# Optimization experiments

Hardware: AMD Instinct MI355X
Metric: run time of the kernel (lower is better)

The kernel has to match this reference:

```python
import jax, jax.numpy as jnp
import numpy as np
from jax import lax

RES = 2048
MAX_VAL = 1.0
COST_SCALE = 0.01
N_ITERS = 10
BOUNDARY_FRAC = 0.02  # sparse scattered Dirichlet cells, realistic for a planner occupancy grid


def _neighbor_sum(V):
    # replicate-pad (zero-Neumann at the outer border), 4-point stencil sum
    Vp = jnp.pad(V, 1, mode='edge')
    return Vp[:-2, 1:-1] + Vp[2:, 1:-1] + Vp[1:-1, :-2] + Vp[1:-1, 2:]


def setup_inputs() -> dict:
    key = jax.random.key(0)
    k1, k2, k3, k4 = jax.random.split(key, 4)
    x = jax.random.uniform(k1, (RES, RES), jnp.float32)
    # sparse boundary/obstacle cells (boundary_types > 0 means Dirichlet cell)
    boundary_types = (jax.random.uniform(k2, (RES, RES)) < BOUNDARY_FRAC).astype(jnp.int32)
    boundary_conditions = jax.random.uniform(k3, (RES, RES), jnp.float32)
    # learnable cost field, initialized around cost_scale (some negatives so ReLU matters)
    C = COST_SCALE + COST_SCALE * jax.random.normal(k4, (RES, RES), jnp.float32)
    return {'x': x, 'C': C, 'boundary_types': boundary_types,
            'boundary_conditions': boundary_conditions}


def reference(x, C, boundary_types, boundary_conditions):
    mask = boundary_types > 0
    # inject boundary conditions into the initial potential (x[obj_inds] = bc[obj_inds])
    V = jnp.where(mask, boundary_conditions, x)
    C_pos = jax.nn.relu(C)
    denom = 4.0 + C_pos  # screened Laplace: (4 + C) V = sum(neighbors)

    def step(V, _):
        V_new = _neighbor_sum(V) / denom
        V_new = jnp.where(mask, boundary_conditions, V_new)
        return V_new, None

    V, _ = lax.scan(step, V, None, length=N_ITERS)

    out = jnp.where(V >= MAX_VAL, 0.95 * MAX_VAL, V)
    out = jnp.where(mask, boundary_conditions, out)
    return out, C_pos
```

## Files before the change

### kernel.cpp

```cpp
#include <hip/hip_runtime.h>


#define RES    2048
#define XHALO  12
#define YHALO  10
#define DIMX   128
#define DIMY   64
#define OUTX   (DIMX - 2*XHALO)
#define OUTY   (DIMY - 2*YHALO)
#define NBX    ((RES + OUTX - 1) / OUTX)
#define NBY    ((RES + OUTY - 1) / OUTY)
#define NWG    (NBX*NBY)
#define NITER  10

__global__ __launch_bounds__(512, 4)
void laplace10_fused(const float* __restrict__ Xin,
                     const float* __restrict__ Cin,
                     const float* __restrict__ BTf,
                     const float* __restrict__ BCin,
                     float* __restrict__ OUT,
                     float* __restrict__ CPOS) {
  __shared__ __align__(16) float V[2][DIMY][DIMX];

  const int t  = threadIdx.x;
  const int q  = t & 31;
  const int ty = t >> 5;
  const int x0 = q * 4;
  const int y0 = ty * 4;

  int wg = (int)blockIdx.x;
  {
    const int qq = NWG / 8, rr = NWG % 8;
    const int xcd = wg % 8, off = wg / 8;
    wg = (xcd < rr ? xcd * (qq + 1) : rr * (qq + 1) + (xcd - rr) * qq) + off;
  }
  const int bx  = wg % NBX, by = wg / NBX;
  const int tx0 = bx * OUTX - XHALO;
  const int ty0 = by * OUTY - YHALO;
  const int gx0 = tx0 + x0;

  const bool xfull = (gx0 >= 0) && (gx0 + 4 <= RES);
  const int  xcl   = (gx0 < 0) ? 0 : (RES - 1);
  const bool xin   = xfull && (x0 >= XHALO) && (x0 < XHALO + OUTX);

  auto load4 = [&](const float* __restrict__ g, int row) -> float4 {
    if (xfull) return *(const float4*)(g + (size_t)row * RES + gx0);
    const float v = g[(size_t)row * RES + xcl];
    return make_float4(v, v, v, v);
  };

  const bool lq0 = (gx0 + 0 <= 0);
  const bool lq1 = (gx0 + 1 <= 0);
  const bool lq2 = (gx0 + 2 <= 0);
  const bool lq3 = (gx0 + 3 <= 0);
  const bool rq0 = (gx0 + 0 >= RES - 1);
  const bool rq1 = (gx0 + 1 >= RES - 1);
  const bool rq2 = (gx0 + 2 >= RES - 1);
  const bool rq3 = (gx0 + 3 >= RES - 1);

  unsigned mb = 0u;
  float4 Bq[4], Rq[4], cur[4];
#pragma unroll
  for (int j = 0; j < 4; ++j) {
    const int yy = y0 + j;
    const int g  = ty0 + yy;
    const int gc = g < 0 ? 0 : (g > RES - 1 ? RES - 1 : g);
    const float4 mv = load4(BTf, gc);
    const float4 bv = load4(BCin, gc);
    const float4 cv = load4(Cin, gc);
    const float4 xv = load4(Xin, gc);
    const unsigned m0 = (__float_as_uint(mv.x) != 0u);
    const unsigned m1 = (__float_as_uint(mv.y) != 0u);
    const unsigned m2 = (__float_as_uint(mv.z) != 0u);
    const unsigned m3 = (__float_as_uint(mv.w) != 0u);
    mb |= (m0 | (m1 << 1) | (m2 << 2) | (m3 << 3)) << (4 * j);
    float4 B;
    B.x = m0 ? bv.x : 0.0f;  B.y = m1 ? bv.y : 0.0f;
    B.z = m2 ? bv.z : 0.0f;  B.w = m3 ? bv.w : 0.0f;
    Bq[j] = B;
    float4 cp;
    cp.x = cv.x > 0.0f ? cv.x : 0.0f;
    cp.y = cv.y > 0.0f ? cv.y : 0.0f;
    cp.z = cv.z > 0.0f ? cv.z : 0.0f;
    cp.w = cv.w > 0.0f ? cv.w : 0.0f;
    float4 R;
    R.x = m0 ? 0.0f : 1.0f / (4.0f + cp.x);
    R.y = m1 ? 0.0f : 1.0f / (4.0f + cp.y);
    R.z = m2 ? 0.0f : 1.0f / (4.0f + cp.z);
    R.w = m3 ? 0.0f : 1.0f / (4.0f + cp.w);
    Rq[j] = R;
    float4 v0;
    v0.x = m0 ? B.x : xv.x;  v0.y = m1 ? B.y : xv.y;
    v0.z = m2 ? B.z : xv.z;  v0.w = m3 ? B.w : xv.w;
    cur[j] = v0;
    *(float4*)(&V[0][yy][x0]) = v0;
    if (xin && yy >= YHALO && yy < YHALO + OUTY && g < RES) {
      *(float4*)(CPOS + (size_t)g * RES + gx0) = cp;
    }
  }
  __syncthreads();

  const int ytop = (ty == 0)  ? 0        : y0 - 1;
  const int ybot = (ty == 15) ? DIMY - 1 : y0 + 4;

  #define ROW_STEP(J, VP, VM, VN, NV)                                          \
    {                                                                          \
      const int g_ = ty0 + y0 + (J);                                           \
      const float lf = __shfl((VM).w, (t + 63) & 63);                          \
      const float rt = __shfl((VM).x, (t + 1) & 63);                           \
      const float4 va = (g_ <= 0)       ? (VM) : (VP);                         \
      const float4 vb = (g_ >= RES - 1) ? (VM) : (VN);                         \
      const float n0 = va.x + vb.x + (lq0 ? (VM).x : lf)     + (rq0 ? (VM).x : (VM).y); \
      const float n1 = va.y + vb.y + (lq1 ? (VM).y : (VM).x) + (rq1 ? (VM).y : (VM).z); \
      const float n2 = va.z + vb.z + (lq2 ? (VM).z : (VM).y) + (rq2 ? (VM).z : (VM).w); \
      const float n3 = va.w + vb.w + (lq3 ? (VM).w : (VM).z) + (rq3 ? (VM).w : rt);     \
      (NV).x = fmaf(n0, Rq[J].x, Bq[J].x);                                     \
      (NV).y = fmaf(n1, Rq[J].y, Bq[J].y);                                     \
      (NV).z = fmaf(n2, Rq[J].z, Bq[J].z);                                     \
      (NV).w = fmaf(n3, Rq[J].w, Bq[J].w);                                     \
    }

#pragma unroll 1
  for (int it = 1; it < NITER; ++it) {
    const float* const src = &V[(it + 1) & 1][0][0];
    float* const dst       = &V[it & 1][0][0];
    const float4 top = *(const float4*)(src + ytop * DIMX + x0);
    const float4 bot = *(const float4*)(src + ybot * DIMX + x0);
    float4 n0v, n1v, n2v, n3v;
    ROW_STEP(0, top,    cur[0], cur[1], n0v);
    ROW_STEP(1, cur[0], cur[1], cur[2], n1v);
    ROW_STEP(2, cur[1], cur[2], cur[3], n2v);
    ROW_STEP(3, cur[2], cur[3], bot,    n3v);
    cur[0] = n0v; cur[1] = n1v; cur[2] = n2v; cur[3] = n3v;
    *(float4*)(dst + (y0 + 0) * DIMX + x0) = n0v;
    *(float4*)(dst + (y0 + 1) * DIMX + x0) = n1v;
    *(float4*)(dst + (y0 + 2) * DIMX + x0) = n2v;
    *(float4*)(dst + (y0 + 3) * DIMX + x0) = n3v;
    __syncthreads();
  }

  {
    const float* const src = &V[1][0][0];
    const float4 top = *(const float4*)(src + ytop * DIMX + x0);
    const float4 bot = *(const float4*)(src + ybot * DIMX + x0);
    float4 n0v, n1v, n2v, n3v;
    ROW_STEP(0, top,    cur[0], cur[1], n0v);
    ROW_STEP(1, cur[0], cur[1], cur[2], n1v);
    ROW_STEP(2, cur[1], cur[2], cur[3], n2v);
    ROW_STEP(3, cur[2], cur[3], bot,    n3v);
    cur[0] = n0v; cur[1] = n1v; cur[2] = n2v; cur[3] = n3v;
#pragma unroll
    for (int j = 0; j < 4; ++j) {
      const int yy = y0 + j;
      const int g  = ty0 + yy;
      if (xin && yy >= YHALO && yy < YHALO + OUTY && g < RES) {
        const float4 nv = cur[j];
        float4 o;
        o.x = (nv.x >= 1.0f) ? 0.95f : nv.x;
        o.y = (nv.y >= 1.0f) ? 0.95f : nv.y;
        o.z = (nv.z >= 1.0f) ? 0.95f : nv.z;
        o.w = (nv.w >= 1.0f) ? 0.95f : nv.w;
        *(float4*)(OUT + (size_t)g * RES + gx0) = o;
      }
    }
  }
  #undef ROW_STEP
}

extern "C" void kernel_launch(void* const* d_in, const int* in_sizes, int n_in,
                              void* d_out, int out_size, void* d_ws, size_t ws_size,
                              hipStream_t stream) {
  const float* Xin  = (const float*)d_in[0];
  const float* Cin  = (const float*)d_in[1];
  const float* BTf  = (const float*)d_in[2];
  const float* BCin = (const float*)d_in[3];
  float* OUT  = (float*)d_out;
  float* CPOS = OUT + (size_t)RES * RES;

  hipLaunchKernelGGL(laplace10_fused, dim3(NWG), dim3(512), 0, stream,
                     Xin, Cin, BTf, BCin, OUT, CPOS);
}
```

Measured before the change: 131.1 us.

## Exchange stencil halos via wave shuffles and small LDS buffer; specialize interior tiles

Replaces the full double-buffered 64x128 LDS tile with a small halo buffer: rows shared between the two half-waves of a wavefront are exchanged with cross-lane shuffles, and only rows crossing wavefront boundaries go through LDS. Interior workgroups use a template specialization that drops all boundary clamping logic. The lower LDS footprint allows raising launch bounds to 8 blocks per CU, and the iteration loop is fully unrolled. This increases register pressure, which could limit the occupancy gain.

```diff
diff --git a/kernel.cpp b/kernel.cpp
--- a/kernel.cpp
+++ b/kernel.cpp
@@ -12,68 +12,64 @@
 #define NBY    ((RES + OUTY - 1) / OUTY)
 #define NWG    (NBX*NBY)
 #define NITER  10
-
-__global__ __launch_bounds__(512, 4)
-void laplace10_fused(const float* __restrict__ Xin,
-                     const float* __restrict__ Cin,
-                     const float* __restrict__ BTf,
-                     const float* __restrict__ BCin,
-                     float* __restrict__ OUT,
-                     float* __restrict__ CPOS) {
-  __shared__ __align__(16) float V[2][DIMY][DIMX];
-
-  const int t  = threadIdx.x;
-  const int q  = t & 31;
-  const int ty = t >> 5;
-  const int x0 = q * 4;
-  const int y0 = ty * 4;
-
-  int wg = (int)blockIdx.x;
-  {
-    const int qq = NWG / 8, rr = NWG % 8;
-    const int xcd = wg % 8, off = wg / 8;
-    wg = (xcd < rr ? xcd * (qq + 1) : rr * (qq + 1) + (xcd - rr) * qq) + off;
-  }
-  const int bx  = wg % NBX, by = wg / NBX;
-  const int tx0 = bx * OUTX - XHALO;
-  const int ty0 = by * OUTY - YHALO;
-  const int gx0 = tx0 + x0;
-
-  const bool xfull = (gx0 >= 0) && (gx0 + 4 <= RES);
-  const int  xcl   = (gx0 < 0) ? 0 : (RES - 1);
+#define HSTRIDE (8*2*DIMX)
+
+using HaloT = float[2][8][2][DIMX];
+
+template<bool EDGE>
+__device__ __forceinline__ void body(const int t, const int bx, const int by,
+    const float* __restrict__ Xin, const float* __restrict__ Cin,
+    const float* __restrict__ BTf, const float* __restrict__ BCin,
+    float* __restrict__ OUT, float* __restrict__ CPOS, HaloT& H)
+{
+  const int  q      = t & 31;
+  const int  ty     = t >> 5;
+  const int  w      = t >> 6;
+  const bool tyEven = (ty & 1) == 0;
+  const int  x0     = q * 4;
+  const int  y0     = ty * 4;
+  const int  tx0    = bx * OUTX - XHALO;
+  const int  ty0    = by * OUTY - YHALO;
+  const int  gx0    = tx0 + x0;
+  const int  gyr    = ty0 + y0;
+
+  const bool xfull = !EDGE || ((gx0 >= 0) && (gx0 + 4 <= RES));
   const bool xin   = xfull && (x0 >= XHALO) && (x0 < XHALO + OUTX);
 
+  const bool lq0 = EDGE && (gx0 + 0 <= 0);
+  const bool lq1 = EDGE && (gx0 + 1 <= 0);
+  const bool lq2 = EDGE && (gx0 + 2 <= 0);
+  const bool lq3 = EDGE && (gx0 + 3 <= 0);
+  const bool rq0 = EDGE && (gx0 + 0 >= RES - 1);
+  const bool rq1 = EDGE && (gx0 + 1 >= RES - 1);
+  const bool rq2 = EDGE && (gx0 + 2 >= RES - 1);
+  const bool rq3 = EDGE && (gx0 + 3 >= RES - 1);
+
   auto load4 = [&](const float* __restrict__ g, int row) -> float4 {
-    if (xfull) return *(const float4*)(g + (size_t)row * RES + gx0);
-    const float v = g[(size_t)row * RES + xcl];
-    return make_float4(v, v, v, v);
+    if constexpr (EDGE) {
+      if (xfull) return *(const float4*)(g + (size_t)row * RES + gx0);
+      const int xc = (gx0 < 0) ? 0 : (RES - 1);
+      const float v = g[(size_t)row * RES + xc];
+      return make_float4(v, v, v, v);
+    } else {
+      return *(const float4*)(g + (size_t)row * RES + gx0);
+    }
   };
 
-  const bool lq0 = (gx0 + 0 <= 0);
-  const bool lq1 = (gx0 + 1 <= 0);
-  const bool lq2 = (gx0 + 2 <= 0);
-  const bool lq3 = (gx0 + 3 <= 0);
-  const bool rq0 = (gx0 + 0 >= RES - 1);
-  const bool rq1 = (gx0 + 1 >= RES - 1);
-  const bool rq2 = (gx0 + 2 >= RES - 1);
-  const bool rq3 = (gx0 + 3 >= RES - 1);
-
-  unsigned mb = 0u;
   float4 Bq[4], Rq[4], cur[4];
 #pragma unroll
   for (int j = 0; j < 4; ++j) {
     const int yy = y0 + j;
-    const int g  = ty0 + yy;
-    const int gc = g < 0 ? 0 : (g > RES - 1 ? RES - 1 : g);
+    const int g  = gyr + j;
+    const int gc = EDGE ? (g < 0 ? 0 : (g > RES - 1 ? RES - 1 : g)) : g;
     const float4 mv = load4(BTf, gc);
     const float4 bv = load4(BCin, gc);
     const float4 cv = load4(Cin, gc);
     const float4 xv = load4(Xin, gc);
-    const unsigned m0 = (__float_as_uint(mv.x) != 0u);
-    const unsigned m1 = (__float_as_uint(mv.y) != 0u);
-    const unsigned m2 = (__float_as_uint(mv.z) != 0u);
-    const unsigned m3 = (__float_as_uint(mv.w) != 0u);
-    mb |= (m0 | (m1 << 1) | (m2 << 2) | (m3 << 3)) << (4 * j);
+    const bool m0 = __float_as_uint(mv.x) != 0u;
+    const bool m1 = __float_as_uint(mv.y) != 0u;
+    const bool m2 = __float_as_uint(mv.z) != 0u;
+    const bool m3 = __float_as_uint(mv.w) != 0u;
     float4 B;
     B.x = m0 ? bv.x : 0.0f;  B.y = m1 ? bv.y : 0.0f;
     B.z = m2 ? bv.z : 0.0f;  B.w = m3 ? bv.w : 0.0f;
@@ -93,78 +89,100 @@
     v0.x = m0 ? B.x : xv.x;  v0.y = m1 ? B.y : xv.y;
     v0.z = m2 ? B.z : xv.z;  v0.w = m3 ? B.w : xv.w;
     cur[j] = v0;
-    *(float4*)(&V[0][yy][x0]) = v0;
-    if (xin && yy >= YHALO && yy < YHALO + OUTY && g < RES) {
+    if (xin && yy >= YHALO && yy < YHALO + OUTY && (!EDGE || g < RES)) {
       *(float4*)(CPOS + (size_t)g * RES + gx0) = cp;
     }
   }
+
+  const int wr = tyEven ? (w > 0 ? w - 1 : 0) : (w < 7 ? w + 1 : 7);
+  float* const       hw = &H[0][w][tyEven ? 0 : 1][x0];
+  const float* const hr = &H[0][wr][tyEven ? 1 : 0][x0];
+  *(float4*)hw = tyEven ? cur[0] : cur[3];
   __syncthreads();
 
-  const int ytop = (ty == 0)  ? 0        : y0 - 1;
-  const int ybot = (ty == 15) ? DIMY - 1 : y0 + 4;
-
-  #define ROW_STEP(J, VP, VM, VN, NV)                                          \
-    {                                                                          \
-      const int g_ = ty0 + y0 + (J);                                           \
-      const float lf = __shfl((VM).w, (t + 63) & 63);                          \
-      const float rt = __shfl((VM).x, (t + 1) & 63);                           \
-      const float4 va = (g_ <= 0)       ? (VM) : (VP);                         \
-      const float4 vb = (g_ >= RES - 1) ? (VM) : (VN);                         \
-      const float n0 = va.x + vb.x + (lq0 ? (VM).x : lf)     + (rq0 ? (VM).x : (VM).y); \
-      const float n1 = va.y + vb.y + (lq1 ? (VM).y : (VM).x) + (rq1 ? (VM).y : (VM).z); \
-      const float n2 = va.z + vb.z + (lq2 ? (VM).z : (VM).y) + (rq2 ? (VM).z : (VM).w); \
-      const float n3 = va.w + vb.w + (lq3 ? (VM).w : (VM).z) + (rq3 ? (VM).w : rt);     \
-      (NV).x = fmaf(n0, Rq[J].x, Bq[J].x);                                     \
-      (NV).y = fmaf(n1, Rq[J].y, Bq[J].y);                                     \
-      (NV).z = fmaf(n2, Rq[J].z, Bq[J].z);                                     \
-      (NV).w = fmaf(n3, Rq[J].w, Bq[J].w);                                     \
-    }
-
-#pragma unroll 1
-  for (int it = 1; it < NITER; ++it) {
-    const float* const src = &V[(it + 1) & 1][0][0];
-    float* const dst       = &V[it & 1][0][0];
-    const float4 top = *(const float4*)(src + ytop * DIMX + x0);
-    const float4 bot = *(const float4*)(src + ybot * DIMX + x0);
-    float4 n0v, n1v, n2v, n3v;
-    ROW_STEP(0, top,    cur[0], cur[1], n0v);
-    ROW_STEP(1, cur[0], cur[1], cur[2], n1v);
-    ROW_STEP(2, cur[1], cur[2], cur[3], n2v);
-    ROW_STEP(3, cur[2], cur[3], bot,    n3v);
-    cur[0] = n0v; cur[1] = n1v; cur[2] = n2v; cur[3] = n3v;
-    *(float4*)(dst + (y0 + 0) * DIMX + x0) = n0v;
-    *(float4*)(dst + (y0 + 1) * DIMX + x0) = n1v;
-    *(float4*)(dst + (y0 + 2) * DIMX + x0) = n2v;
-    *(float4*)(dst + (y0 + 3) * DIMX + x0) = n3v;
-    __syncthreads();
-  }
-
+  auto rowstep = [&](int gy, const float4 R, const float4 B,
+                     const float4 vp, const float4 vm, const float4 vn) -> float4 {
+    const float lf = __shfl(vm.w, (t + 63) & 63);
+    const float rt = __shfl(vm.x, (t + 1) & 63);
+    float4 nv;
+    if constexpr (EDGE) {
+      const float4 va = (gy <= 0)       ? vm : vp;
+      const float4 vb = (gy >= RES - 1) ? vm : vn;
+      nv.x = fmaf(va.x + vb.x + (lq0 ? vm.x : lf)   + (rq0 ? vm.x : vm.y), R.x, B.x);
+      nv.y = fmaf(va.y + vb.y + (lq1 ? vm.y : vm.x) + (rq1 ? vm.y : vm.z), R.y, B.y);
+      nv.z = fmaf(va.z + vb.z + (lq2 ? vm.z : vm.y) + (rq2 ? vm.z : vm.w), R.z, B.z);
+      nv.w = fmaf(va.w + vb.w + (lq3 ? vm.w : vm.z) + (rq3 ? vm.w : rt),   R.w, B.w);
+    } else {
+      nv.x = fmaf(vp.x + vn.x + lf   + vm.y, R.x, B.x);
+      nv.y = fmaf(vp.y + vn.y + vm.x + vm.z, R.y, B.y);
+      nv.z = fmaf(vp.z + vn.z + vm.y + vm.w, R.z, B.z);
+      nv.w = fmaf(vp.w + vn.w + vm.z + rt,   R.w, B.w);
+    }
+    return nv;
+  };
+
+#pragma unroll
+  for (int it = 1; it <= NITER; ++it) {
+    const int src = (it - 1) & 1;
+    const float4 snd = tyEven ? cur[3] : cur[0];
+    float4 oth;
+    oth.x = __shfl(snd.x, t ^ 32);
+    oth.y = __shfl(snd.y, t ^ 32);
+    oth.z = __shfl(snd.z, t ^ 32);
+    oth.w = __shfl(snd.w, t ^ 32);
+    const float4 hv = *(const float4*)(hr + src * HSTRIDE);
+    const float4 P0 = tyEven ? hv : oth;
+    const float4 P3 = tyEven ? oth : hv;
+    const float4 n0 = rowstep(gyr + 0, Rq[0], Bq[0], P0,     cur[0], cur[1]);
+    const float4 n1 = rowstep(gyr + 1, Rq[1], Bq[1], cur[0], cur[1], cur[2]);
+    const float4 n2 = rowstep(gyr + 2, Rq[2], Bq[2], cur[1], cur[2], cur[3]);
+    const float4 n3 = rowstep(gyr + 3, Rq[3], Bq[3], cur[2], cur[3], P3);
+    cur[0] = n0; cur[1] = n1; cur[2] = n2; cur[3] = n3;
+    if (it < NITER) {
+      *(float4*)(hw + (it & 1) * HSTRIDE) = tyEven ? n0 : n3;
+      __syncthreads();
+    }
+  }
+
+#pragma unroll
+  for (int j = 0; j < 4; ++j) {
+    const int yy = y0 + j;
+    const int g  = gyr + j;
+    if (xin && yy >= YHALO && yy < YHALO + OUTY && (!EDGE || g < RES)) {
+      const float4 nv = cur[j];
+      float4 o;
+      o.x = (nv.x >= 1.0f) ? 0.95f : nv.x;
+      o.y = (nv.y >= 1.0f) ? 0.95f : nv.y;
+      o.z = (nv.z >= 1.0f) ? 0.95f : nv.z;
+      o.w = (nv.w >= 1.0f) ? 0.95f : nv.w;
+      *(float4*)(OUT + (size_t)g * RES + gx0) = o;
+    }
+  }
+}
+
+__global__ __launch_bounds__(512, 8)
+void laplace10_fused(const float* __restrict__ Xin,
+                     const float* __restrict__ Cin,
+                     const float* __restrict__ BTf,
+                     const float* __restrict__ BCin,
+                     float* __restrict__ OUT,
+                     float* __restrict__ CPOS) {
+  __shared__ __align__(16) float H[2][8][2][DIMX];
+
+  const int t = threadIdx.x;
+  int wg = (int)blockIdx.x;
   {
-    const float* const src = &V[1][0][0];
-    const float4 top = *(const float4*)(src + ytop * DIMX + x0);
-    const float4 bot = *(const float4*)(src + ybot * DIMX + x0);
-    float4 n0v, n1v, n2v, n3v;
-    ROW_STEP(0, top,    cur[0], cur[1], n0v);
-    ROW_STEP(1, cur[0], cur[1], cur[2], n1v);
-    ROW_STEP(2, cur[1], cur[2], cur[3], n2v);
-    ROW_STEP(3, cur[2], cur[3], bot,    n3v);
-    cur[0] = n0v; cur[1] = n1v; cur[2] = n2v; cur[3] = n3v;
-#pragma unroll
-    for (int j = 0; j < 4; ++j) {
-      const int yy = y0 + j;
-      const int g  = ty0 + yy;
-      if (xin && yy >= YHALO && yy < YHALO + OUTY && g < RES) {
-        const float4 nv = cur[j];
-        float4 o;
-        o.x = (nv.x >= 1.0f) ? 0.95f : nv.x;
-        o.y = (nv.y >= 1.0f) ? 0.95f : nv.y;
-        o.z = (nv.z >= 1.0f) ? 0.95f : nv.z;
-        o.w = (nv.w >= 1.0f) ? 0.95f : nv.w;
-        *(float4*)(OUT + (size_t)g * RES + gx0) = o;
-      }
-    }
-  }
-  #undef ROW_STEP
+    const int qq = NWG / 8, rr = NWG % 8;
+    const int xcd = wg % 8, off = wg / 8;
+    wg = (xcd < rr ? xcd * (qq + 1) : rr * (qq + 1) + (xcd - rr) * qq) + off;
+  }
+  const int bx = wg % NBX, by = wg / NBX;
+
+  if (bx > 0 && bx < NBX - 1 && by > 0 && by < NBY - 1) {
+    body<false>(t, bx, by, Xin, Cin, BTf, BCin, OUT, CPOS, H);
+  } else {
+    body<true>(t, bx, by, Xin, Cin, BTf, BCin, OUT, CPOS, H);
+  }
 }
 
 extern "C" void kernel_launch(void* const* d_in, const int* in_sizes, int n_in,
```

Result: slower. 342.8 us (+161.4%).
